# Optimization experiments

Hardware: AMD Instinct MI355X
Metric: run time of the kernel (lower is better)

The kernel has to match this reference:

```python
import jax, jax.numpy as jnp
import numpy as np

B, N, FIN, H, D = 2, 512, 128, 4, 64
NEG_SLOPE = 0.2


def setup_inputs() -> dict:
    key = jax.random.key(0)
    ks = jax.random.split(key, 5)
    x = jax.random.normal(ks[0], (B, N, FIN), dtype=jnp.float32)
    # xavier-ish scaled params
    W_proj = jax.random.normal(ks[1], (H, FIN, D), dtype=jnp.float32) * (1.0 / np.sqrt(FIN + D))
    b_proj = jnp.zeros((H, D), dtype=jnp.float32)
    W_cat_weight = jax.random.normal(ks[2], (H, D, 2 * D), dtype=jnp.float32) * (1.0 / np.sqrt(3 * D))
    W_cat_bias = jnp.zeros((H, D), dtype=jnp.float32)
    a = jax.random.normal(ks[3], (H, D), dtype=jnp.float32) * (1.0 / np.sqrt(D))
    bias_param = jnp.zeros((H * D,), dtype=jnp.float32)
    return {"x": x, "W_proj": W_proj, "b_proj": b_proj,
            "W_cat_weight": W_cat_weight, "W_cat_bias": W_cat_bias,
            "a": a, "bias_param": bias_param}


def reference(x, W_proj, b_proj, W_cat_weight, W_cat_bias, a, bias_param):
    # h[b,h,n,d] = W^h x_n + b^h
    h = jnp.einsum('bni,hid->bhnd', x, W_proj) + b_proj[None, :, None, :]
    d = h.shape[-1]
    # W_cat [h_i || h_j] == W1 h_i + W2 h_j  (avoids O(N^2*2D) concat tensor)
    W1 = W_cat_weight[:, :, :d]   # (H, D, D) acts on source node i
    W2 = W_cat_weight[:, :, d:]   # (H, D, D) acts on target node j
    zi = jnp.einsum('bhnd,hed->bhne', h, W1)  # (B,H,N,D)
    zj = jnp.einsum('bhnd,hed->bhne', h, W2)  # (B,H,N,D)
    # z[b,h,i,j,e] = zi[b,h,i,e] + zj[b,h,j,e] + bias, then LeakyReLU
    z = zi[:, :, :, None, :] + zj[:, :, None, :, :] + W_cat_bias[None, :, None, None, :]
    z = jnp.where(z >= 0, z, NEG_SLOPE * z)
    # e[b,h,i,j] = a_h . z
    e = jnp.einsum('bhije,he->bhij', z, a)
    attn = jax.nn.softmax(e, axis=-1)          # softmax over neighbors j
    out = jnp.einsum('bhij,bhjd->bhid', attn, h)  # (B,H,N,D)
    b_, h_, n_, d_ = out.shape
    out = out.transpose(0, 2, 1, 3).reshape(b_, n_, h_ * d_)  # concat heads
    out = out + bias_param
    return out
```

## Files before the change

kernel.cpp:

```cpp
#include <hip/hip_runtime.h>
#include <hip/hip_bf16.h>

#define NN 512
#define FIN 128
#define HH 4
#define DD 64
#define SW 68


__global__ void prep_kernel(const float* __restrict__ a, float* __restrict__ sgn,
                            float* __restrict__ pa, int* __restrict__ src)
{
    int h = threadIdx.x;
    if (h >= HH) return;
    const float* ah = a + h * DD;
    int np = 0;
    for (int e = 0; e < DD; ++e) if (ah[e] >= 0.f) ++np;
    int GP = (np + 3) >> 2;
    for (int s = 0; s < SW; ++s) { src[h*SW+s] = 0; pa[h*SW+s] = 0.f; }
    int ip = 0, in_ = 4 * GP;
    for (int e = 0; e < DD; ++e) {
        float v = ah[e];
        int s = (v >= 0.f) ? (ip++) : (in_++);
        src[h*SW+s] = e; pa[h*SW+s] = fabsf(v);
    }
    for (int g = 0; g < 17; ++g) sgn[h*17+g] = (g < GP) ? 0.4f : -0.4f;
}

__global__ __launch_bounds__(256) void proj_kernel(
    const float* __restrict__ x, const float* __restrict__ Wp,
    const float* __restrict__ bp, const float* __restrict__ Wc,
    const float* __restrict__ Wcb, const float* __restrict__ a,
    const float* __restrict__ pa_ws, const int* __restrict__ src_ws,
    float* __restrict__ h_ws, float* __restrict__ azi_ws, float* __restrict__ azj_ws,
    float* __restrict__ adi_ws, float* __restrict__ adj_ws)
{
    int blk = blockIdx.x;
    int bh = blk >> 6;
    int n0 = (blk & 63) << 3;
    int b = bh >> 2, hh = bh & 3;

    __shared__ float xs[8 * FIN];
    __shared__ float hs[8][DD];
    __shared__ float Wcs[DD][2 * DD + 1];
    __shared__ float tzi[8][DD];
    __shared__ float tzj[8][DD];

    int t = threadIdx.x;

    ((float4*)xs)[t] = ((const float4*)(x + ((size_t)b * NN + n0) * FIN))[t];
    {
        const float4* wg = (const float4*)(Wc + (size_t)hh * DD * 2 * DD);
        #pragma unroll
        for (int k = 0; k < 8; ++k) {
            int idx = t + 256 * k;
            int r = idx >> 5, c4 = (idx & 31) * 4;
            float4 v = wg[idx];
            Wcs[r][c4] = v.x; Wcs[r][c4 + 1] = v.y;
            Wcs[r][c4 + 2] = v.z; Wcs[r][c4 + 3] = v.w;
        }
    }
    __syncthreads();

    int d = t & 63, w = t >> 6;
    const float* Wph = Wp + (size_t)hh * FIN * DD;
    float bpv = bp[hh * DD + d];
    float acc0 = bpv, acc1 = bpv;
    #pragma unroll 8
    for (int i = 0; i < FIN; ++i) {
        float wv = Wph[i * DD + d];
        acc0 = fmaf(xs[w * FIN + i], wv, acc0);
        acc1 = fmaf(xs[(w + 4) * FIN + i], wv, acc1);
    }
    hs[w][d] = acc0; hs[w + 4][d] = acc1;
    float* hg = h_ws + ((size_t)bh * NN + n0) * DD;
    hg[w * DD + d] = acc0; hg[(w + 4) * DD + d] = acc1;
    __syncthreads();

    int e = d;
    float zb = Wcb[hh * DD + e];
    float zi0 = zb, zi1 = zb, zj0 = 0.f, zj1 = 0.f;
    #pragma unroll 8
    for (int d2 = 0; d2 < DD; ++d2) {
        float w1 = Wcs[e][d2];
        float w2 = Wcs[e][DD + d2];
        float h0 = hs[w][d2], h1 = hs[w + 4][d2];
        zi0 = fmaf(h0, w1, zi0); zi1 = fmaf(h1, w1, zi1);
        zj0 = fmaf(h0, w2, zj0); zj1 = fmaf(h1, w2, zj1);
    }
    tzi[w][e] = zi0; tzi[w + 4][e] = zi1;
    tzj[w][e] = zj0; tzj[w + 4][e] = zj1;

    float av = a[hh * DD + e];
    float p0 = av * zi0, p1 = av * zi1, q0 = av * zj0, q1 = av * zj1;
    #pragma unroll
    for (int off = 32; off; off >>= 1) {
        p0 += __shfl_xor(p0, off); p1 += __shfl_xor(p1, off);
        q0 += __shfl_xor(q0, off); q1 += __shfl_xor(q1, off);
    }
    if (e == 0) {
        adi_ws[bh * NN + n0 + w]     = 0.6f * p0;
        adi_ws[bh * NN + n0 + w + 4] = 0.6f * p1;
        adj_ws[bh * NN + n0 + w]     = 0.6f * q0;
        adj_ws[bh * NN + n0 + w + 4] = 0.6f * q1;
    }
    __syncthreads();

    {
        int r = t >> 5, sl = t & 31;
        const int*   sh = src_ws + hh * SW;
        const float* ph = pa_ws + hh * SW;
        float* azib = azi_ws + ((size_t)bh * NN + n0) * SW;
        float* azjb = azj_ws + ((size_t)bh * NN + n0) * SW;
        for (int s = sl; s < SW; s += 32) {
            int se = sh[s]; float pav = ph[s];
            azib[(size_t)r * SW + s] = pav * tzi[r][se];
            azjb[(size_t)r * SW + s] = pav * tzj[r][se];
        }
    }
}

__global__ __launch_bounds__(256) void attn_kernel(
    const float* __restrict__ h_ws, const float* __restrict__ azi_ws,
    const float* __restrict__ azj_ws, const float* __restrict__ adi_ws,
    const float* __restrict__ adj_ws, const float* __restrict__ sgn_ws,
    float* __restrict__ pacc, float* __restrict__ pm, float* __restrict__ ps)
{
    int blk = blockIdx.x;
    int js = blk & 7, it = (blk >> 3) & 7, bh = blk >> 6;
    int j0 = js << 6, i0 = it << 6, hh = bh & 3;

    __shared__ float azis[64 * SW];
    __shared__ float buf[64][SW];

    int t = threadIdx.x, lane = t & 63;
    int w = __builtin_amdgcn_readfirstlane(t >> 6);

    {
        const float4* srcp = (const float4*)(azi_ws + ((size_t)bh * NN + i0) * SW);
        float4* dst = (float4*)azis;
        #pragma unroll
        for (int k = 0; k < 5; ++k) {
            int idx = t + 256 * k;
            if (idx < 64 * SW / 4) dst[idx] = srcp[idx];
        }
    }

    float4 azj[17];
    {
        const float4* src4 = (const float4*)(azj_ws + ((size_t)bh * NN + j0 + lane) * SW);
        #pragma unroll
        for (int k = 0; k < 17; ++k) azj[k] = src4[k];
    }
    float adjv = adj_ws[bh * NN + j0 + lane];
    float sgn[17];
    {
        const float* sg = sgn_ws + hh * 17;
        #pragma unroll
        for (int k = 0; k < 17; ++k) sgn[k] = sg[k];
    }
    const float* adib = adi_ws + bh * NN + i0;

    __syncthreads();

    float pmk = 0.f, psk = 0.f;
    #pragma unroll 2
    for (int ii = 0; ii < 16; ++ii) {
        int i = 16 * w + ii;
        const float4* arow = (const float4*)(azis + i * SW);
        float acc0 = 0.f, acc1 = 0.f;
        #pragma unroll
        for (int k = 0; k < 17; ++k) {
            float4 zi4 = arow[k];
            float s = sgn[k];
            acc0 = fmaf(s, __builtin_fabsf(zi4.x + azj[k].x), acc0);
            acc1 = fmaf(s, __builtin_fabsf(zi4.y + azj[k].y), acc1);
            acc0 = fmaf(s, __builtin_fabsf(zi4.z + azj[k].z), acc0);
            acc1 = fmaf(s, __builtin_fabsf(zi4.w + azj[k].w), acc1);
        }
        float e = adib[i] + adjv + acc0 + acc1;
        float m = e;
        #pragma unroll
        for (int off = 32; off; off >>= 1) m = fmaxf(m, __shfl_xor(m, off));
        float p = __expf(e - m);
        float ssum = p;
        #pragma unroll
        for (int off = 32; off; off >>= 1) ssum += __shfl_xor(ssum, off);
        buf[i][lane] = p;
        pmk = (lane == ii) ? m : pmk;
        psk = (lane == ii) ? ssum : psk;
    }

    float hreg[64];
    {
        const float* hb = h_ws + ((size_t)bh * NN + j0) * DD + lane;
        #pragma unroll
        for (int j = 0; j < 64; ++j) hreg[j] = hb[j * DD];
    }

    size_t obase = ((size_t)(js * 8 + bh) * NN + i0) * DD + lane;
    #pragma unroll 2
    for (int ii = 0; ii < 16; ++ii) {
        int i = 16 * w + ii;
        const float4* prow = (const float4*)buf[i];
        float a0 = 0.f, a1 = 0.f;
        #pragma unroll
        for (int k = 0; k < 16; ++k) {
            float4 p4 = prow[k];
            a0 = fmaf(p4.x, hreg[4 * k + 0], a0);
            a1 = fmaf(p4.y, hreg[4 * k + 1], a1);
            a0 = fmaf(p4.z, hreg[4 * k + 2], a0);
            a1 = fmaf(p4.w, hreg[4 * k + 3], a1);
        }
        pacc[obase + (size_t)i * DD] = a0 + a1;
    }
    if (lane < 16) {
        int r = (js * 8 + bh) * NN + i0 + 16 * w + lane;
        pm[r] = pmk; ps[r] = psk;
    }
}

__global__ __launch_bounds__(256) void combine_kernel(
    const float* __restrict__ pacc, const float* __restrict__ pm,
    const float* __restrict__ ps, const float* __restrict__ bias_param,
    float* __restrict__ out)
{
    int tid = blockIdx.x * 256 + threadIdx.x;
    int d = tid & 63;
    int row = tid >> 6;
    int bh = row >> 9, n = row & 511;
    int b = bh >> 2, hh = bh & 3;
    float mv[8];
    float m = -1e30f;
    #pragma unroll
    for (int p = 0; p < 8; ++p) { mv[p] = pm[p * 4096 + row]; m = fmaxf(m, mv[p]); }
    float denom = 0.f, acc = 0.f;
    #pragma unroll
    for (int p = 0; p < 8; ++p) {
        float wgt = __expf(mv[p] - m);
        denom = fmaf(ps[p * 4096 + row], wgt, denom);
        acc = fmaf(pacc[(size_t)p * 262144 + (size_t)row * 64 + d], wgt, acc);
    }
    out[((size_t)b * NN + n) * (HH * DD) + hh * DD + d] =
        acc / denom + bias_param[hh * DD + d];
}

extern "C" void kernel_launch(void* const* d_in, const int* in_sizes, int n_in,
                              void* d_out, int out_size, void* d_ws, size_t ws_size,
                              hipStream_t stream) {
    const float* x    = (const float*)d_in[0];
    const float* Wp   = (const float*)d_in[1];
    const float* bp   = (const float*)d_in[2];
    const float* Wc   = (const float*)d_in[3];
    const float* Wcb  = (const float*)d_in[4];
    const float* a    = (const float*)d_in[5];
    const float* bpar = (const float*)d_in[6];
    float* out = (float*)d_out;

    float* ws     = (float*)d_ws;
    float* h_ws   = ws;
    float* azi_ws = ws + 262144;
    float* azj_ws = ws + 540672;
    float* adi_ws = ws + 819200;
    float* adj_ws = ws + 823296;
    float* pacc   = ws + 827392;
    float* pm     = ws + 2924544;
    float* ps     = ws + 2957312;
    float* sgn_ws = ws + 2990080;
    float* pa_ws  = ws + 2990148;
    int*   src_ws = (int*)(ws + 2990420);

    prep_kernel<<<dim3(1), dim3(64), 0, stream>>>(a, sgn_ws, pa_ws, src_ws);
    proj_kernel<<<dim3(512), dim3(256), 0, stream>>>(
        x, Wp, bp, Wc, Wcb, a, pa_ws, src_ws,
        h_ws, azi_ws, azj_ws, adi_ws, adj_ws);
    attn_kernel<<<dim3(512), dim3(256), 0, stream>>>(
        h_ws, azi_ws, azj_ws, adi_ws, adj_ws, sgn_ws, pacc, pm, ps);
    combine_kernel<<<dim3(1024), dim3(256), 0, stream>>>(
        pacc, pm, ps, bpar, out);
}
```

Before: 50.18 us.

## Drop prep kernel, compute sign permutation in-wave, shrink attention tiles to 8 rows

The separate single-block prep kernel is removed. The sign-sorted slot permutation of `a` is now computed with a wave ballot/popcount inside the projection kernel and the attention kernel, so the shared-memory staging step and one launch go away. The attention kernel now processes 8 query rows per block instead of 64, giving 4096 blocks, and stages the h tile in shared memory instead of 64 registers per thread. This is meant to raise occupancy and parallelism and cut launch overhead. In exchange, each azj row and h tile is reloaded by eight times as many blocks, which adds global and L2 traffic.

After: 44.75 us. 1.12x faster.

```diff
diff --git a/kernel.cpp b/kernel.cpp
--- a/kernel.cpp
+++ b/kernel.cpp
@@ -8,30 +8,10 @@
 #define SW 68
 
 
-__global__ void prep_kernel(const float* __restrict__ a, float* __restrict__ sgn,
-                            float* __restrict__ pa, int* __restrict__ src)
-{
-    int h = threadIdx.x;
-    if (h >= HH) return;
-    const float* ah = a + h * DD;
-    int np = 0;
-    for (int e = 0; e < DD; ++e) if (ah[e] >= 0.f) ++np;
-    int GP = (np + 3) >> 2;
-    for (int s = 0; s < SW; ++s) { src[h*SW+s] = 0; pa[h*SW+s] = 0.f; }
-    int ip = 0, in_ = 4 * GP;
-    for (int e = 0; e < DD; ++e) {
-        float v = ah[e];
-        int s = (v >= 0.f) ? (ip++) : (in_++);
-        src[h*SW+s] = e; pa[h*SW+s] = fabsf(v);
-    }
-    for (int g = 0; g < 17; ++g) sgn[h*17+g] = (g < GP) ? 0.4f : -0.4f;
-}
-
 __global__ __launch_bounds__(256) void proj_kernel(
     const float* __restrict__ x, const float* __restrict__ Wp,
     const float* __restrict__ bp, const float* __restrict__ Wc,
     const float* __restrict__ Wcb, const float* __restrict__ a,
-    const float* __restrict__ pa_ws, const int* __restrict__ src_ws,
     float* __restrict__ h_ws, float* __restrict__ azi_ws, float* __restrict__ azj_ws,
     float* __restrict__ adi_ws, float* __restrict__ adj_ws)
 {
@@ -43,8 +23,6 @@
     __shared__ float xs[8 * FIN];
     __shared__ float hs[8][DD];
     __shared__ float Wcs[DD][2 * DD + 1];
-    __shared__ float tzi[8][DD];
-    __shared__ float tzj[8][DD];
 
     int t = threadIdx.x;
 
@@ -62,22 +40,21 @@
     }
     __syncthreads();
 
-    int d = t & 63, w = t >> 6;
+    int e = t & 63, w = t >> 6;
     const float* Wph = Wp + (size_t)hh * FIN * DD;
-    float bpv = bp[hh * DD + d];
+    float bpv = bp[hh * DD + e];
     float acc0 = bpv, acc1 = bpv;
     #pragma unroll 8
     for (int i = 0; i < FIN; ++i) {
-        float wv = Wph[i * DD + d];
+        float wv = Wph[i * DD + e];
         acc0 = fmaf(xs[w * FIN + i], wv, acc0);
         acc1 = fmaf(xs[(w + 4) * FIN + i], wv, acc1);
     }
-    hs[w][d] = acc0; hs[w + 4][d] = acc1;
+    hs[w][e] = acc0; hs[w + 4][e] = acc1;
     float* hg = h_ws + ((size_t)bh * NN + n0) * DD;
-    hg[w * DD + d] = acc0; hg[(w + 4) * DD + d] = acc1;
+    hg[w * DD + e] = acc0; hg[(w + 4) * DD + e] = acc1;
     __syncthreads();
 
-    int e = d;
     float zb = Wcb[hh * DD + e];
     float zi0 = zb, zi1 = zb, zj0 = 0.f, zj1 = 0.f;
     #pragma unroll 8
@@ -88,8 +65,6 @@
         zi0 = fmaf(h0, w1, zi0); zi1 = fmaf(h1, w1, zi1);
         zj0 = fmaf(h0, w2, zj0); zj1 = fmaf(h1, w2, zj1);
     }
-    tzi[w][e] = zi0; tzi[w + 4][e] = zi1;
-    tzj[w][e] = zj0; tzj[w + 4][e] = zj1;
 
     float av = a[hh * DD + e];
     float p0 = av * zi0, p1 = av * zi1, q0 = av * zj0, q1 = av * zj1;
@@ -104,69 +79,77 @@
         adj_ws[bh * NN + n0 + w]     = 0.6f * q0;
         adj_ws[bh * NN + n0 + w + 4] = 0.6f * q1;
     }
-    __syncthreads();
-
-    {
-        int r = t >> 5, sl = t & 31;
-        const int*   sh = src_ws + hh * SW;
-        const float* ph = pa_ws + hh * SW;
-        float* azib = azi_ws + ((size_t)bh * NN + n0) * SW;
-        float* azjb = azj_ws + ((size_t)bh * NN + n0) * SW;
-        for (int s = sl; s < SW; s += 32) {
-            int se = sh[s]; float pav = ph[s];
-            azib[(size_t)r * SW + s] = pav * tzi[r][se];
-            azjb[(size_t)r * SW + s] = pav * tzj[r][se];
-        }
+
+    unsigned long long mask = __ballot(av >= 0.f);
+    int np = __popcll(mask);
+    int GP = (np + 3) >> 2;
+    int below = __popcll(mask & ((1ull << e) - 1ull));
+    int slot = (av >= 0.f) ? below : (4 * GP + (e - below));
+    float pav = __builtin_fabsf(av);
+
+    float* azib = azi_ws + ((size_t)bh * NN + n0) * SW;
+    float* azjb = azj_ws + ((size_t)bh * NN + n0) * SW;
+    azib[w * SW + slot]       = pav * zi0;
+    azib[(w + 4) * SW + slot] = pav * zi1;
+    azjb[w * SW + slot]       = pav * zj0;
+    azjb[(w + 4) * SW + slot] = pav * zj1;
+    int p1c = 4 * GP - np;
+    if (e < 4) {
+        int psl = (e < p1c) ? (np + e) : (4 * GP + 64 - np + (e - p1c));
+        azib[w * SW + psl] = 0.f; azib[(w + 4) * SW + psl] = 0.f;
+        azjb[w * SW + psl] = 0.f; azjb[(w + 4) * SW + psl] = 0.f;
     }
 }
 
 __global__ __launch_bounds__(256) void attn_kernel(
     const float* __restrict__ h_ws, const float* __restrict__ azi_ws,
     const float* __restrict__ azj_ws, const float* __restrict__ adi_ws,
-    const float* __restrict__ adj_ws, const float* __restrict__ sgn_ws,
+    const float* __restrict__ adj_ws, const float* __restrict__ a,
     float* __restrict__ pacc, float* __restrict__ pm, float* __restrict__ ps)
 {
     int blk = blockIdx.x;
-    int js = blk & 7, it = (blk >> 3) & 7, bh = blk >> 6;
-    int j0 = js << 6, i0 = it << 6, hh = bh & 3;
-
-    __shared__ float azis[64 * SW];
-    __shared__ float buf[64][SW];
+    int js = blk & 7, it = (blk >> 3) & 63, bh = blk >> 9;
+    int j0 = js << 6, i0 = it << 3, hh = bh & 3;
+
+    __shared__ float azis[8 * SW];
+    __shared__ float pbuf[8][64];
+    __shared__ float htile[64 * 64];
 
     int t = threadIdx.x, lane = t & 63;
-    int w = __builtin_amdgcn_readfirstlane(t >> 6);
-
+    int w = t >> 6;
+
+    if (t < 136)
+        ((float4*)azis)[t] = ((const float4*)(azi_ws + ((size_t)bh * NN + i0) * SW))[t];
     {
-        const float4* srcp = (const float4*)(azi_ws + ((size_t)bh * NN + i0) * SW);
-        float4* dst = (float4*)azis;
-        #pragma unroll
-        for (int k = 0; k < 5; ++k) {
-            int idx = t + 256 * k;
-            if (idx < 64 * SW / 4) dst[idx] = srcp[idx];
-        }
+        const float4* hsrc = (const float4*)(h_ws + ((size_t)bh * NN + j0) * DD);
+        float4* hdst = (float4*)htile;
+        #pragma unroll
+        for (int k = 0; k < 4; ++k) hdst[t + 256 * k] = hsrc[t + 256 * k];
     }
 
     float4 azj[17];
     {
-        const float4* src4 = (const float4*)(azj_ws + ((size_t)bh * NN + j0 + lane) * SW);
-        #pragma unroll
-        for (int k = 0; k < 17; ++k) azj[k] = src4[k];
+        const float4* srcj = (const float4*)(azj_ws + ((size_t)bh * NN + j0 + lane) * SW);
+        #pragma unroll
+        for (int k = 0; k < 17; ++k) azj[k] = srcj[k];
     }
     float adjv = adj_ws[bh * NN + j0 + lane];
+
+    float av_e = a[hh * DD + lane];
+    unsigned long long mask = __ballot(av_e >= 0.f);
+    int GP = (__popcll(mask) + 3) >> 2;
     float sgn[17];
-    {
-        const float* sg = sgn_ws + hh * 17;
-        #pragma unroll
-        for (int k = 0; k < 17; ++k) sgn[k] = sg[k];
-    }
-    const float* adib = adi_ws + bh * NN + i0;
+    #pragma unroll
+    for (int k = 0; k < 17; ++k) sgn[k] = (k < GP) ? 0.4f : -0.4f;
+
+    float adiA = adi_ws[bh * NN + i0 + 2 * w];
+    float adiB = adi_ws[bh * NN + i0 + 2 * w + 1];
 
     __syncthreads();
 
-    float pmk = 0.f, psk = 0.f;
-    #pragma unroll 2
-    for (int ii = 0; ii < 16; ++ii) {
-        int i = 16 * w + ii;
+    #pragma unroll
+    for (int ii = 0; ii < 2; ++ii) {
+        int i = 2 * w + ii;
         const float4* arow = (const float4*)(azis + i * SW);
         float acc0 = 0.f, acc1 = 0.f;
         #pragma unroll
@@ -178,46 +161,39 @@
             acc0 = fmaf(s, __builtin_fabsf(zi4.z + azj[k].z), acc0);
             acc1 = fmaf(s, __builtin_fabsf(zi4.w + azj[k].w), acc1);
         }
-        float e = adib[i] + adjv + acc0 + acc1;
-        float m = e;
+        float ev = ((ii == 0) ? adiA : adiB) + adjv + acc0 + acc1;
+        float m = ev;
         #pragma unroll
         for (int off = 32; off; off >>= 1) m = fmaxf(m, __shfl_xor(m, off));
-        float p = __expf(e - m);
+        float p = __expf(ev - m);
         float ssum = p;
         #pragma unroll
         for (int off = 32; off; off >>= 1) ssum += __shfl_xor(ssum, off);
-        buf[i][lane] = p;
-        pmk = (lane == ii) ? m : pmk;
-        psk = (lane == ii) ? ssum : psk;
-    }
-
-    float hreg[64];
-    {
-        const float* hb = h_ws + ((size_t)bh * NN + j0) * DD + lane;
-        #pragma unroll
-        for (int j = 0; j < 64; ++j) hreg[j] = hb[j * DD];
-    }
-
-    size_t obase = ((size_t)(js * 8 + bh) * NN + i0) * DD + lane;
-    #pragma unroll 2
-    for (int ii = 0; ii < 16; ++ii) {
-        int i = 16 * w + ii;
-        const float4* prow = (const float4*)buf[i];
-        float a0 = 0.f, a1 = 0.f;
-        #pragma unroll
-        for (int k = 0; k < 16; ++k) {
-            float4 p4 = prow[k];
-            a0 = fmaf(p4.x, hreg[4 * k + 0], a0);
-            a1 = fmaf(p4.y, hreg[4 * k + 1], a1);
-            a0 = fmaf(p4.z, hreg[4 * k + 2], a0);
-            a1 = fmaf(p4.w, hreg[4 * k + 3], a1);
+        pbuf[i][lane] = p;
+        if (lane == 0) {
+            pm[(js * 8 + bh) * NN + i0 + i] = m;
+            ps[(js * 8 + bh) * NN + i0 + i] = ssum;
         }
-        pacc[obase + (size_t)i * DD] = a0 + a1;
-    }
-    if (lane < 16) {
-        int r = (js * 8 + bh) * NN + i0 + 16 * w + lane;
-        pm[r] = pmk; ps[r] = psk;
-    }
+    }
+
+    float accA = 0.f, accB = 0.f;
+    const float4* pA = (const float4*)pbuf[2 * w];
+    const float4* pB = (const float4*)pbuf[2 * w + 1];
+    #pragma unroll
+    for (int k = 0; k < 16; ++k) {
+        float4 a4 = pA[k], b4 = pB[k];
+        float h0 = htile[(4 * k + 0) * 64 + lane];
+        float h1 = htile[(4 * k + 1) * 64 + lane];
+        float h2 = htile[(4 * k + 2) * 64 + lane];
+        float h3 = htile[(4 * k + 3) * 64 + lane];
+        accA = fmaf(a4.x, h0, accA); accB = fmaf(b4.x, h0, accB);
+        accA = fmaf(a4.y, h1, accA); accB = fmaf(b4.y, h1, accB);
+        accA = fmaf(a4.z, h2, accA); accB = fmaf(b4.z, h2, accB);
+        accA = fmaf(a4.w, h3, accA); accB = fmaf(b4.w, h3, accB);
+    }
+    size_t ob = ((size_t)(js * 8 + bh) * NN + i0 + 2 * w) * DD + lane;
+    pacc[ob] = accA;
+    pacc[ob + DD] = accB;
 }
 
 __global__ __launch_bounds__(256) void combine_kernel(
@@ -266,16 +242,11 @@
     float* pacc   = ws + 827392;
     float* pm     = ws + 2924544;
     float* ps     = ws + 2957312;
-    float* sgn_ws = ws + 2990080;
-    float* pa_ws  = ws + 2990148;
-    int*   src_ws = (int*)(ws + 2990420);
-
-    prep_kernel<<<dim3(1), dim3(64), 0, stream>>>(a, sgn_ws, pa_ws, src_ws);
+
     proj_kernel<<<dim3(512), dim3(256), 0, stream>>>(
-        x, Wp, bp, Wc, Wcb, a, pa_ws, src_ws,
-        h_ws, azi_ws, azj_ws, adi_ws, adj_ws);
-    attn_kernel<<<dim3(512), dim3(256), 0, stream>>>(
-        h_ws, azi_ws, azj_ws, adi_ws, adj_ws, sgn_ws, pacc, pm, ps);
+        x, Wp, bp, Wc, Wcb, a, h_ws, azi_ws, azj_ws, adi_ws, adj_ws);
+    attn_kernel<<<dim3(4096), dim3(256), 0, stream>>>(
+        h_ws, azi_ws, azj_ws, adi_ws, adj_ws, a, pacc, pm, ps);
     combine_kernel<<<dim3(1024), dim3(256), 0, stream>>>(
         pacc, pm, ps, bpar, out);
 }
```
